# Performance work log

Hardware: AMD Instinct MI355X
Metric: run time of the kernel (lower is better)

## Reference

```python
import jax, jax.numpy as jnp
import numpy as np
import math


def _mirror_even(x):
    # even-symmetric extension: [..., H, W] -> [..., 2H, 2W]
    x = jnp.concatenate([x, jnp.flip(x, -1)], axis=-1)
    return jnp.concatenate([x, jnp.flip(x, -2)], axis=-2)


def _grad_img(x):
    # Fourier-domain spectral gradient on the even-symmetric extension,
    # matching PoissonCompositionLayer.grad_img (wx = arange(1,2W+1)-(W+1) = arange(-W,W)).
    H, W = x.shape[-2], x.shape[-1]
    kx = jnp.arange(-W, W)[None, :]          # [1, 2W]
    ky = jnp.arange(-H, H)[:, None]          # [2H, 1]
    dft = jnp.fft.fftshift(jnp.fft.fft2(_mirror_even(x)), axes=(-1, -2))
    gx = jnp.fft.ifft2(jnp.fft.fftshift((2j * math.pi / (2 * W)) * kx * dft, axes=(-1, -2))).real
    gy = jnp.fft.ifft2(jnp.fft.fftshift((2j * math.pi / (2 * H)) * ky * dft, axes=(-1, -2))).real
    return gx[..., :H, :W], gy[..., :H, :W]


def setup_inputs() -> dict:
    key = jax.random.key(0)
    k1, k2, k3 = jax.random.split(key, 3)
    B, C, H, W = 2, 3, 512, 512
    target = jax.random.normal(k1, (B, C, H, W), dtype=jnp.float32)
    source = jax.random.normal(k2, (B, C, H, W), dtype=jnp.float32)
    mask = jax.random.uniform(k3, (B, C, H, W), dtype=jnp.float32)
    return {"target": target, "source": source, "mask": mask}


def reference(target, source, mask):
    H, W = target.shape[-2], target.shape[-1]
    # composite gradient field
    gxt, gyt = _grad_img(target)
    gxs, gys = _grad_img(source)
    gx = (1.0 - mask) * gxt + mask * gxs
    gy = (1.0 - mask) * gyt + mask * gys
    # odd extension in x / even in y for gx; odd in y / even in x for gy
    gxp = jnp.concatenate([gx, -jnp.flip(gx, -1)], axis=-1)
    gxp = jnp.concatenate([gxp, jnp.flip(gxp, -2)], axis=-2)
    gyp = jnp.concatenate([gy, -jnp.flip(gy, -2)], axis=-2)
    gyp = jnp.concatenate([gyp, jnp.flip(gyp, -1)], axis=-1)
    dx = jnp.fft.fftshift(jnp.fft.fft2(gxp), axes=(-1, -2))
    dy = jnp.fft.fftshift(jnp.fft.fft2(gyp), axes=(-1, -2))
    # shifted frequency grids (DC sits at index [H, W])
    kx = jnp.arange(-W, W)[None, :]
    ky = jnp.arange(-H, H)[:, None]
    fx = 2j * math.pi * kx / (2 * W)
    fy = 2j * math.pi * ky / (2 * H)
    coeff = (fx * dx + fy * dy) / (fx ** 2 + fy ** 2 + 1e-10)
    coeff = coeff.at[..., H, W].set(0.0)  # zero DC component
    u = jnp.fft.ifft2(jnp.fft.fftshift(coeff, axes=(-1, -2)))
    res = u.real[..., :H, :W]
    # mean-matching on the unmasked region; original uses batch index 0's means for all batches
    inv = 1.0 - mask
    denom = jnp.sum(inv, axis=(-1, -2))                       # [B, C]
    mean1 = jnp.sum(target * inv, axis=(-1, -2)) / denom      # [B, C]
    mean2 = jnp.sum(res * inv, axis=(-1, -2)) / denom         # [B, C]
    return res + (mean1[0] - mean2[0])[None, :, None, None]
```

## Files before the change

kernel.cpp:

```cpp
#include <hip/hip_runtime.h>


#define CH 262144
#define NCH 6
#define NTOT (NCH*CH)

typedef _Float16 f16x8 __attribute__((ext_vector_type(8)));
typedef float f32x4  __attribute__((ext_vector_type(4)));

static constexpr float kPi        = 3.14159265358979323846f;
static constexpr float kPiOver512 = 0.006135923151542565f;
static constexpr float kPi2Norm   = 3.7649933338155804e-05f;
static constexpr float kInvHW     = 3.814697265625e-06f;

__device__ __forceinline__ void hst(float v, short* p) {
    *reinterpret_cast<_Float16*>(p) = (_Float16)v;
}

__device__ __forceinline__ float hfun(int k) {
    if (k == 0) return 0.f;
    float sgn = 1.f;
    if (k < 0) { k = -k; sgn = -1.f; }
    if (k > 512) { k = 1024 - k; sgn = -sgn; }
    float sv, cv;
    sincosf((float)k * (kPi / 1024.0f), &sv, &cv);
    float v = cv / sv;
    if (k & 1) v = -v;
    return sgn * v;
}

__device__ __forceinline__ void gl_lds16(const short* g, const short* l) {
    __builtin_amdgcn_global_load_lds(
        (const __attribute__((address_space(1))) void*)g,
        (__attribute__((address_space(3))) void*)l, 16, 0, 0);
}

#define FOFF(r, j) (((r) << 6) + 8 * ((j) ^ ((r) & 7)))
#define MFMA16(a, b, c) __builtin_amdgcn_mfma_f32_16x16x32_f16(a, b, c, 0, 0, 0)

template<int OM, int TA>
__global__ __launch_bounds__(256) void gemm_tn(
    const short* __restrict__ T0, const short* __restrict__ X0, int sX0,
    float* __restrict__ Cf0, short* __restrict__ O0, int sC0,
    const short* __restrict__ T1, const short* __restrict__ X1, int sX1,
    float* __restrict__ Cf1, short* __restrict__ O1, int sC1,
    int zsplit, const float* __restrict__ msk, float* __restrict__ redp)
{
    __shared__ short LS[2][4352];
    int z = blockIdx.z;
    const short *T, *X; float* Cf; short* O;
    if (z < zsplit) {
        T = T0; X = X0 + (size_t)z * sX0;
        Cf = Cf0 ? Cf0 + (size_t)z * sC0 : nullptr;
        O  = O0 ? O0 + (size_t)z * sC0 : nullptr;
    } else {
        int zz = z - zsplit;
        T = T1; X = X1 + (size_t)zz * sX1;
        Cf = Cf1 ? Cf1 + (size_t)zz * sC1 : nullptr;
        O  = O1 ? O1 + (size_t)zz * sC1 : nullptr;
    }
    int tid = threadIdx.x;
    int l = tid & 63, w = tid >> 6;
    int m0 = blockIdx.y * 64, n0 = blockIdx.x * 64;

    int xbase = TA ? n0 : m0;
    int srow = w * 8 + (l >> 3);
    int skc  = (l & 7) ^ ((l >> 3) & 7);
    const short* gX = X + (size_t)(xbase + srow) * 512 + 8 * skc;

    int wr = w >> 1, wc = w & 1;
    int lr = l & 15, lc = l >> 4;
    int rX0 = (TA ? wc : wr) * 32 + lr, rX1 = rX0 + 16;
    int ttb = (TA ? (m0 + wr * 32) : (n0 + wc * 32)) >> 4;
    const short* Tw0 = T + (size_t)ttb * 8192 + l * 8;
    const short* Tw1 = Tw0 + 8192;

    f32x4 a00 = {0,0,0,0}, a01 = a00, a10 = a00, a11 = a00;

#define STAGE_X(nb, k0) \
    gl_lds16(gX + (k0), &LS[nb][w * 512]); \
    gl_lds16(gX + (k0) + 32 * 512, &LS[nb][w * 512 + 2048]);

    STAGE_X(0, 0)
    __syncthreads();

    for (int step = 0; step < 8; ++step) {
        int buf = step & 1;
        if (step < 7) { STAGE_X(buf ^ 1, (step + 1) * 64) }
#pragma unroll
        for (int ks = 0; ks < 2; ++ks) {
            int j = lc + 4 * ks;
            int kc = step * 2 + ks;
            f16x8 xf0 = *(const f16x8*)&LS[buf][FOFF(rX0, j)];
            f16x8 xf1 = *(const f16x8*)&LS[buf][FOFF(rX1, j)];
            f16x8 tf0 = *(const f16x8*)(Tw0 + kc * 512);
            f16x8 tf1 = *(const f16x8*)(Tw1 + kc * 512);
            if constexpr (TA) {
                a00 = MFMA16(tf0, xf0, a00);
                a01 = MFMA16(tf0, xf1, a01);
                a10 = MFMA16(tf1, xf0, a10);
                a11 = MFMA16(tf1, xf1, a11);
            } else {
                a00 = MFMA16(xf0, tf0, a00);
                a01 = MFMA16(xf0, tf1, a01);
                a10 = MFMA16(xf1, tf0, a10);
                a11 = MFMA16(xf1, tf1, a11);
            }
        }
        __syncthreads();
    }
#undef STAGE_X

    int crow = m0 + wr * 32 + lc * 4;
    int ccol = n0 + wc * 32 + lr;
    const f32x4* accs[2][2] = {{&a00, &a01}, {&a10, &a11}};
    float lsum = 0.f;
#pragma unroll
    for (int q = 0; q < 2; ++q)
#pragma unroll
        for (int pp = 0; pp < 2; ++pp)
#pragma unroll
            for (int rr = 0; rr < 4; ++rr) {
                int idx = (crow + q * 16 + rr) * 512 + ccol + pp * 16;
                float v = (*accs[q][pp])[rr];
                if (OM == 1) {
                    hst(v, O + idx);
                } else {
                    Cf[idx] = v;
                    lsum += v * (1.0f - msk[(size_t)z * CH + idx]);
                }
            }
    if (OM == 2) {
        float* red = (float*)LS;
        red[tid] = lsum;
        __syncthreads();
        for (int s2 = 128; s2 > 0; s2 >>= 1) {
            if (tid < s2) red[tid] += red[tid + s2];
            __syncthreads();
        }
        if (tid == 0) redp[z * 64 + blockIdx.y * 8 + blockIdx.x] = red[0];
    }
}

__global__ __launch_bounds__(256) void gemm_l1(
    const short* __restrict__ dn, const short* __restrict__ dt,
    const short* __restrict__ GT, const float* __restrict__ msk,
    short* __restrict__ C_, short* __restrict__ D_)
{
    __shared__ short LS[2][4352];
    int z = blockIdx.z;
    bool gxp = z < 6;
    int zz = gxp ? z : z - 6;
    const short* X = (gxp ? dn : dt) + (size_t)zz * CH;
    const float* mz = msk + (size_t)zz * CH;

    int tid = threadIdx.x;
    int l = tid & 63, w = tid >> 6;
    int m0 = blockIdx.y * 64, n0 = blockIdx.x * 64;

    int srow = w * 8 + (l >> 3);
    int skc  = (l & 7) ^ ((l >> 3) & 7);
    const short* gX = X + (size_t)(m0 + srow) * 512 + 8 * skc;

    int wr = w >> 1, wc = w & 1;
    int lr = l & 15, lc = l >> 4;
    int rX0 = wr * 32 + lr, rX1 = rX0 + 16;
    int ttb = (n0 + wc * 32) >> 4;
    const short* Tw0 = GT + (size_t)ttb * 8192 + l * 8;
    const short* Tw1 = Tw0 + 8192;

    f32x4 a00 = {0,0,0,0}, a01 = a00, a10 = a00, a11 = a00;

#define STAGE_X(nb, k0) \
    gl_lds16(gX + (k0), &LS[nb][w * 512]); \
    gl_lds16(gX + (k0) + 32 * 512, &LS[nb][w * 512 + 2048]);

    STAGE_X(0, 0)
    __syncthreads();

    for (int step = 0; step < 8; ++step) {
        int buf = step & 1;
        if (step < 7) { STAGE_X(buf ^ 1, (step + 1) * 64) }
#pragma unroll
        for (int ks = 0; ks < 2; ++ks) {
            int j = lc + 4 * ks;
            int kc = step * 2 + ks;
            f16x8 xf0 = *(const f16x8*)&LS[buf][FOFF(rX0, j)];
            f16x8 xf1 = *(const f16x8*)&LS[buf][FOFF(rX1, j)];
            f16x8 tf0 = *(const f16x8*)(Tw0 + kc * 512);
            f16x8 tf1 = *(const f16x8*)(Tw1 + kc * 512);
            a00 = MFMA16(xf0, tf0, a00);
            a01 = MFMA16(xf0, tf1, a01);
            a10 = MFMA16(xf1, tf0, a10);
            a11 = MFMA16(xf1, tf1, a11);
        }
        __syncthreads();
    }
#undef STAGE_X

    const f32x4* accs[2][2] = {{&a00, &a01}, {&a10, &a11}};
    float* tile = (float*)LS;

    if (gxp) {
        short* o = C_ + (size_t)zz * CH;
#pragma unroll
        for (int q = 0; q < 2; ++q)
#pragma unroll
            for (int pp = 0; pp < 2; ++pp)
#pragma unroll
                for (int rr = 0; rr < 4; ++rr) {
                    int r = wr * 32 + lc * 4 + q * 16 + rr;
                    int c = wc * 32 + pp * 16 + lr;
                    float v = (*accs[q][pp])[rr] * mz[(size_t)(m0 + r) * 512 + n0 + c];
                    tile[c * 65 + r] = v;
                }
        __syncthreads();
#pragma unroll
        for (int pass = 0; pass < 16; ++pass) {
            int jj = pass * 4 + (tid >> 6);
            int ii = tid & 63;
            hst(tile[jj * 65 + ii], o + (n0 + jj) * 512 + m0 + ii);
        }
    } else {
        short* o = D_ + (size_t)zz * CH;
#pragma unroll
        for (int pass = 0; pass < 16; ++pass) {
            int ii = pass * 4 + (tid >> 6);
            int jj = tid & 63;
            tile[jj * 65 + ii] = mz[(size_t)(n0 + ii) * 512 + m0 + jj];
        }
        __syncthreads();
#pragma unroll
        for (int q = 0; q < 2; ++q)
#pragma unroll
            for (int pp = 0; pp < 2; ++pp)
#pragma unroll
                for (int rr = 0; rr < 4; ++rr) {
                    int r = wr * 32 + lc * 4 + q * 16 + rr;
                    int c = wc * 32 + pp * 16 + lr;
                    float v = (*accs[q][pp])[rr] * tile[r * 65 + c];
                    hst(v, o + (m0 + r) * 512 + n0 + c);
                }
    }
}

__global__ __launch_bounds__(256) void gemm_l3(
    const short* __restrict__ Ms, const short* __restrict__ Mc,
    const short* __restrict__ P, const short* __restrict__ Q,
    short* __restrict__ O_)
{
    __shared__ short LS[2][2][4096];
    int z = blockIdx.z;
    const short* pz = P + (size_t)z * CH;
    const short* qz = Q + (size_t)z * CH;
    short* o = O_ + (size_t)z * CH;

    int tid = threadIdx.x;
    int l = tid & 63, w = tid >> 6;
    int m0 = blockIdx.y * 64, n0 = blockIdx.x * 64;

    int srow = w * 8 + (l >> 3);
    int skc  = (l & 7) ^ ((l >> 3) & 7);
    const short* gP = pz + (size_t)(n0 + srow) * 512 + 8 * skc;
    const short* gQ = qz + (size_t)(n0 + srow) * 512 + 8 * skc;

    int wr = w >> 1, wc = w & 1;
    int lr = l & 15, lc = l >> 4;
    int rB0 = wc * 32 + lr, rB1 = rB0 + 16;
    int ttb = (m0 + wr * 32) >> 4;
    const short* ms0p = Ms + (size_t)ttb * 8192 + l * 8;
    const short* ms1p = ms0p + 8192;
    const short* mc0p = Mc + (size_t)ttb * 8192 + l * 8;
    const short* mc1p = mc0p + 8192;

    f32x4 x00 = {0,0,0,0}, x01 = x00, x10 = x00, x11 = x00;
    f32x4 y00 = x00, y01 = x00, y10 = x00, y11 = x00;

#define STAGE_PQ(nb, k0) \
    gl_lds16(gP + (k0), &LS[nb][0][w * 512]); \
    gl_lds16(gP + (k0) + 32 * 512, &LS[nb][0][w * 512 + 2048]); \
    gl_lds16(gQ + (k0), &LS[nb][1][w * 512]); \
    gl_lds16(gQ + (k0) + 32 * 512, &LS[nb][1][w * 512 + 2048]);

    STAGE_PQ(0, 0)
    __syncthreads();

    for (int step = 0; step < 8; ++step) {
        int buf = step & 1;
        if (step < 7) { STAGE_PQ(buf ^ 1, (step + 1) * 64) }
#pragma unroll
        for (int ks = 0; ks < 2; ++ks) {
            int j = lc + 4 * ks;
            int kc = step * 2 + ks;
            f16x8 p0 = *(const f16x8*)&LS[buf][0][FOFF(rB0, j)];
            f16x8 p1 = *(const f16x8*)&LS[buf][0][FOFF(rB1, j)];
            f16x8 s0 = *(const f16x8*)(ms0p + kc * 512);
            f16x8 s1 = *(const f16x8*)(ms1p + kc * 512);
            x00 = MFMA16(s0, p0, x00);
            x01 = MFMA16(s0, p1, x01);
            x10 = MFMA16(s1, p0, x10);
            x11 = MFMA16(s1, p1, x11);
            f16x8 q0 = *(const f16x8*)&LS[buf][1][FOFF(rB0, j)];
            f16x8 q1 = *(const f16x8*)&LS[buf][1][FOFF(rB1, j)];
            f16x8 c0 = *(const f16x8*)(mc0p + kc * 512);
            f16x8 c1 = *(const f16x8*)(mc1p + kc * 512);
            y00 = MFMA16(c0, q0, y00);
            y01 = MFMA16(c0, q1, y01);
            y10 = MFMA16(c1, q0, y10);
            y11 = MFMA16(c1, q1, y11);
        }
        __syncthreads();
    }
#undef STAGE_PQ

    int crow = m0 + wr * 32 + lc * 4;
    int ccol = n0 + wc * 32 + lr;
    const f32x4* xs[2][2] = {{&x00, &x01}, {&x10, &x11}};
    const f32x4* ys[2][2] = {{&y00, &y01}, {&y10, &y11}};
#pragma unroll
    for (int q = 0; q < 2; ++q)
#pragma unroll
        for (int pp = 0; pp < 2; ++pp) {
            int u = ccol + pp * 16;
            float eu = (u ? 2.0f : 1.0f) * kInvHW;
#pragma unroll
            for (int rr = 0; rr < 4; ++rr) {
                int v = crow + q * 16 + rr;
                float gx = (*xs[q][pp])[rr];
                float gy = (*ys[q][pp])[rr];
                float num = kPiOver512 * ((float)v * gx + (float)u * gy);
                float den = 1e-10f - kPi2Norm * (float)(u * u + v * v);
                float eps = (v ? 2.0f : 1.0f) * eu;
                hst(eps * num / den, o + v * 512 + u);
            }
        }
}

__global__ __launch_bounds__(256) void diff_split_tab(
    const float* __restrict__ s, const float* __restrict__ t, const float* __restrict__ m,
    short* __restrict__ dn, short* __restrict__ dt,
    short* __restrict__ Mc, short* __restrict__ Ms,
    short* __restrict__ McT, short* __restrict__ GT,
    float* __restrict__ mt, float* __restrict__ mi)
{
    int z = blockIdx.z;
    if (z == 6) {
        int bid = blockIdx.y * 16 + blockIdx.x;
        if (bid >= 128) return;
        int g = bid * 256 + threadIdx.x;
        int f = g >> 6, lane = g & 63;
        int r  = ((f >> 4) << 4) | (lane & 15);
        int kb = ((f & 15) << 5) | ((lane >> 4) << 3);
        f16x8 vmc, vms, vmct, vgt;
#pragma unroll
        for (int e = 0; e < 8; ++e) {
            int k = kb + e;
            int p1 = (r * (2 * k + 1)) & 2047;
            float s1, c1; sincosf((float)p1 * (kPi / 1024.0f), &s1, &c1);
            int p2 = (k * (2 * r + 1)) & 2047;
            float s2, c2; sincosf((float)p2 * (kPi / 1024.0f), &s2, &c2);
            float gt = (kPi / 1024.0f) * (hfun(r + k + 1) + hfun(r - k));
            vmc[e]  = (_Float16)c1;
            vms[e]  = (_Float16)s1;
            vmct[e] = (_Float16)c2;
            vgt[e]  = (_Float16)gt;
        }
        *(f16x8*)(Mc  + (size_t)g * 8) = vmc;
        *(f16x8*)(Ms  + (size_t)g * 8) = vms;
        *(f16x8*)(McT + (size_t)g * 8) = vmct;
        *(f16x8*)(GT  + (size_t)g * 8) = vgt;
        return;
    }

    __shared__ float tile[32][33];
    __shared__ float red[512];
    const float* sz = s + (size_t)z * CH;
    const float* tz = t + (size_t)z * CH;
    const float* mz = m + (size_t)z * CH;
    short* nh = dn + (size_t)z * CH;
    short* th = dt + (size_t)z * CH;
    int bx = blockIdx.x * 32, by = blockIdx.y * 32;
    int tx = threadIdx.x & 31, ty = threadIdx.x >> 5;
    float accT = 0.f, accI = 0.f;
    for (int r = ty; r < 32; r += 8) {
        int idx = (by + r) * 512 + bx + tx;
        float tv = tz[idx];
        float d = sz[idx] - tv;
        tile[r][tx] = d;
        hst(d, nh + idx);
        accT += tv;
        if (z < 3) accI += 1.0f - mz[idx];
    }
    __syncthreads();
    for (int r = ty; r < 32; r += 8) {
        hst(tile[tx][r], th + (bx + r) * 512 + by + tx);
    }
    int tid = threadIdx.x;
    red[tid] = accT; red[256 + tid] = accI;
    __syncthreads();
    for (int s2 = 128; s2 > 0; s2 >>= 1) {
        if (tid < s2) { red[tid] += red[tid + s2]; red[256 + tid] += red[256 + tid + s2]; }
        __syncthreads();
    }
    if (tid == 0) {
        int tileid = blockIdx.y * 16 + blockIdx.x;
        mt[z * 256 + tileid] = red[0];
        if (z < 3) mi[z * 256 + tileid] = red[256];
    }
}

__global__ __launch_bounds__(256) void final_out(
    const float* __restrict__ t, const float* __restrict__ U,
    const float* __restrict__ part, float* __restrict__ out)
{
    __shared__ float mtv[6], wmuv[3];
    int tid = threadIdx.x;
    if (tid < 6) {
        float s2 = 0.f;
        for (int k = 0; k < 256; ++k) s2 += part[tid * 256 + k];
        mtv[tid] = s2 * (1.0f / (float)CH);
    }
    if (tid >= 8 && tid < 11) {
        int c = tid - 8;
        float si = 0.f, su = 0.f;
        for (int k = 0; k < 256; ++k) si += part[1536 + c * 256 + k];
        for (int k = 0; k < 64; ++k) su += part[2304 + c * 64 + k];
        wmuv[c] = su / si;
    }
    __syncthreads();
    int n4 = NTOT / 4;
    for (int i = blockIdx.x * blockDim.x + tid; i < n4; i += gridDim.x * blockDim.x) {
        int z = i >> 16;
        int c = z % 3;
        float sh = -mtv[z] + mtv[c] - wmuv[c];
        float4 tv = ((const float4*)t)[i];
        float4 uv = ((const float4*)U)[i];
        ((float4*)out)[i] = make_float4(tv.x + uv.x + sh, tv.y + uv.y + sh,
                                        tv.z + uv.z + sh, tv.w + uv.w + sh);
    }
}

extern "C" void kernel_launch(void* const* d_in, const int* in_sizes, int n_in,
                              void* d_out, int out_size, void* d_ws, size_t ws_size,
                              hipStream_t stream) {
    const float* t = (const float*)d_in[0];
    const float* s = (const float*)d_in[1];
    const float* m = (const float*)d_in[2];
    float* out = (float*)d_out;
    float* F = (float*)d_ws;
    if (ws_size < (size_t)(21 * CH + 4096) * sizeof(float)) return;

    short* T = (short*)F;
    short *Mc = T, *Ms = T + (size_t)CH, *McT = T + 2 * (size_t)CH, *GT = T + 3 * (size_t)CH;
    short* A_ = (short*)(F + 2  * (size_t)CH);
    short* B_ = (short*)(F + 5  * (size_t)CH);
    short* C_ = (short*)(F + 8  * (size_t)CH);
    short* D_ = (short*)(F + 11 * (size_t)CH);
    float* F0  = F + 14 * (size_t)CH;
    float* part = F + 20 * (size_t)CH;

    diff_split_tab<<<dim3(16, 16, 7), 256, 0, stream>>>(s, t, m, A_, B_,
                                                        Mc, Ms, McT, GT,
                                                        part, part + 1536);

    gemm_l1<<<dim3(8, 8, 12), 256, 0, stream>>>(A_, B_, GT, m, C_, D_);

    gemm_tn<1, 1><<<dim3(8, 8, 12), 256, 0, stream>>>(
        Mc, C_, CH, nullptr, A_, CH,
        Ms, D_, CH, nullptr, B_, CH, 6, nullptr, nullptr);

    gemm_l3<<<dim3(8, 8, 6), 256, 0, stream>>>(Ms, Mc, A_, B_, C_);

    gemm_tn<1, 1><<<dim3(8, 8, 6), 256, 0, stream>>>(
        McT, C_, CH, nullptr, D_, CH,
        McT, C_, CH, nullptr, D_, CH, 6, nullptr, nullptr);

    gemm_tn<2, 0><<<dim3(8, 8, 6), 256, 0, stream>>>(
        McT, D_, CH, F0, nullptr, CH,
        McT, D_, CH, F0, nullptr, CH, 6, m, part + 2304);

    final_out<<<768, 256, 0, stream>>>(t, F0, part, out);
}
```

Baseline: 77.95 us.

## Prefetch twiddle fragments one step ahead and remap blocks across XCDs

In the three MFMA GEMM kernels, the global loads of the constant transform-matrix fragments move one K-step ahead into registers, so they overlap with the current step's MFMAs instead of sitting in the critical path. The step loop is also fully unrolled. A new XCD-aware block remap reassigns linear workgroup IDs so consecutive tiles land on the same XCD, which should improve L2 reuse of shared operands. The cost is higher register pressure from the extra prefetch registers. The LDS buffer in gemm_tn also shrinks slightly.

```diff
diff --git a/kernel.cpp b/kernel.cpp
--- a/kernel.cpp
+++ b/kernel.cpp
@@ -29,6 +29,16 @@
     return sgn * v;
 }
 
+__device__ __forceinline__ void xcd_remap(int& bx, int& by, int& bz) {
+    int nx = gridDim.x, ny = gridDim.y;
+    int nwg = nx * ny * gridDim.z;
+    int w = blockIdx.x + nx * (blockIdx.y + ny * blockIdx.z);
+    int s = (w & 7) * (nwg >> 3) + (w >> 3);
+    bx = s % nx; s /= nx;
+    by = s % ny;
+    bz = s / ny;
+}
+
 __device__ __forceinline__ void gl_lds16(const short* g, const short* l) {
     __builtin_amdgcn_global_load_lds(
         (const __attribute__((address_space(1))) void*)g,
@@ -46,8 +56,9 @@
     float* __restrict__ Cf1, short* __restrict__ O1, int sC1,
     int zsplit, const float* __restrict__ msk, float* __restrict__ redp)
 {
-    __shared__ short LS[2][4352];
-    int z = blockIdx.z;
+    __shared__ short LS[2][4096];
+    int bx, by, z;
+    xcd_remap(bx, by, z);
     const short *T, *X; float* Cf; short* O;
     if (z < zsplit) {
         T = T0; X = X0 + (size_t)z * sX0;
@@ -61,7 +72,7 @@
     }
     int tid = threadIdx.x;
     int l = tid & 63, w = tid >> 6;
-    int m0 = blockIdx.y * 64, n0 = blockIdx.x * 64;
+    int m0 = by * 64, n0 = bx * 64;
 
     int xbase = TA ? n0 : m0;
     int srow = w * 8 + (l >> 3);
@@ -82,32 +93,57 @@
     gl_lds16(gX + (k0) + 32 * 512, &LS[nb][w * 512 + 2048]);
 
     STAGE_X(0, 0)
+    f16x8 ct00 = *(const f16x8*)(Tw0);
+    f16x8 ct01 = *(const f16x8*)(Tw0 + 512);
+    f16x8 ct10 = *(const f16x8*)(Tw1);
+    f16x8 ct11 = *(const f16x8*)(Tw1 + 512);
     __syncthreads();
 
+#pragma unroll
     for (int step = 0; step < 8; ++step) {
         int buf = step & 1;
-        if (step < 7) { STAGE_X(buf ^ 1, (step + 1) * 64) }
-#pragma unroll
-        for (int ks = 0; ks < 2; ++ks) {
-            int j = lc + 4 * ks;
-            int kc = step * 2 + ks;
-            f16x8 xf0 = *(const f16x8*)&LS[buf][FOFF(rX0, j)];
-            f16x8 xf1 = *(const f16x8*)&LS[buf][FOFF(rX1, j)];
-            f16x8 tf0 = *(const f16x8*)(Tw0 + kc * 512);
-            f16x8 tf1 = *(const f16x8*)(Tw1 + kc * 512);
+        f16x8 nt00, nt01, nt10, nt11;
+        if (step < 7) {
+            STAGE_X(buf ^ 1, (step + 1) * 64)
+            const short* tn0 = Tw0 + (2 * step + 2) * 512;
+            const short* tn1 = Tw1 + (2 * step + 2) * 512;
+            nt00 = *(const f16x8*)(tn0);
+            nt01 = *(const f16x8*)(tn0 + 512);
+            nt10 = *(const f16x8*)(tn1);
+            nt11 = *(const f16x8*)(tn1 + 512);
+        }
+        {
+            f16x8 x0 = *(const f16x8*)&LS[buf][FOFF(rX0, lc)];
+            f16x8 x1 = *(const f16x8*)&LS[buf][FOFF(rX1, lc)];
             if constexpr (TA) {
-                a00 = MFMA16(tf0, xf0, a00);
-                a01 = MFMA16(tf0, xf1, a01);
-                a10 = MFMA16(tf1, xf0, a10);
-                a11 = MFMA16(tf1, xf1, a11);
+                a00 = MFMA16(ct00, x0, a00);
+                a01 = MFMA16(ct00, x1, a01);
+                a10 = MFMA16(ct10, x0, a10);
+                a11 = MFMA16(ct10, x1, a11);
             } else {
-                a00 = MFMA16(xf0, tf0, a00);
-                a01 = MFMA16(xf0, tf1, a01);
-                a10 = MFMA16(xf1, tf0, a10);
-                a11 = MFMA16(xf1, tf1, a11);
+                a00 = MFMA16(x0, ct00, a00);
+                a01 = MFMA16(x0, ct10, a01);
+                a10 = MFMA16(x1, ct00, a10);
+                a11 = MFMA16(x1, ct10, a11);
             }
         }
-        __syncthreads();
+        {
+            f16x8 x0 = *(const f16x8*)&LS[buf][FOFF(rX0, lc + 4)];
+            f16x8 x1 = *(const f16x8*)&LS[buf][FOFF(rX1, lc + 4)];
+            if constexpr (TA) {
+                a00 = MFMA16(ct01, x0, a00);
+                a01 = MFMA16(ct01, x1, a01);
+                a10 = MFMA16(ct11, x0, a10);
+                a11 = MFMA16(ct11, x1, a11);
+            } else {
+                a00 = MFMA16(x0, ct01, a00);
+                a01 = MFMA16(x0, ct11, a01);
+                a10 = MFMA16(x1, ct01, a10);
+                a11 = MFMA16(x1, ct11, a11);
+            }
+        }
+        __syncthreads();
+        if (step < 7) { ct00 = nt00; ct01 = nt01; ct10 = nt10; ct11 = nt11; }
     }
 #undef STAGE_X
 
@@ -138,7 +174,7 @@
             if (tid < s2) red[tid] += red[tid + s2];
             __syncthreads();
         }
-        if (tid == 0) redp[z * 64 + blockIdx.y * 8 + blockIdx.x] = red[0];
+        if (tid == 0) redp[z * 64 + by * 8 + bx] = red[0];
     }
 }
 
@@ -148,7 +184,8 @@
     short* __restrict__ C_, short* __restrict__ D_)
 {
     __shared__ short LS[2][4352];
-    int z = blockIdx.z;
+    int bx, by, z;
+    xcd_remap(bx, by, z);
     bool gxp = z < 6;
     int zz = gxp ? z : z - 6;
     const short* X = (gxp ? dn : dt) + (size_t)zz * CH;
@@ -156,7 +193,7 @@
 
     int tid = threadIdx.x;
     int l = tid & 63, w = tid >> 6;
-    int m0 = blockIdx.y * 64, n0 = blockIdx.x * 64;
+    int m0 = by * 64, n0 = bx * 64;
 
     int srow = w * 8 + (l >> 3);
     int skc  = (l & 7) ^ ((l >> 3) & 7);
@@ -176,25 +213,43 @@
     gl_lds16(gX + (k0) + 32 * 512, &LS[nb][w * 512 + 2048]);
 
     STAGE_X(0, 0)
+    f16x8 ct00 = *(const f16x8*)(Tw0);
+    f16x8 ct01 = *(const f16x8*)(Tw0 + 512);
+    f16x8 ct10 = *(const f16x8*)(Tw1);
+    f16x8 ct11 = *(const f16x8*)(Tw1 + 512);
     __syncthreads();
 
+#pragma unroll
     for (int step = 0; step < 8; ++step) {
         int buf = step & 1;
-        if (step < 7) { STAGE_X(buf ^ 1, (step + 1) * 64) }
-#pragma unroll
-        for (int ks = 0; ks < 2; ++ks) {
-            int j = lc + 4 * ks;
-            int kc = step * 2 + ks;
-            f16x8 xf0 = *(const f16x8*)&LS[buf][FOFF(rX0, j)];
-            f16x8 xf1 = *(const f16x8*)&LS[buf][FOFF(rX1, j)];
-            f16x8 tf0 = *(const f16x8*)(Tw0 + kc * 512);
-            f16x8 tf1 = *(const f16x8*)(Tw1 + kc * 512);
-            a00 = MFMA16(xf0, tf0, a00);
-            a01 = MFMA16(xf0, tf1, a01);
-            a10 = MFMA16(xf1, tf0, a10);
-            a11 = MFMA16(xf1, tf1, a11);
-        }
-        __syncthreads();
+        f16x8 nt00, nt01, nt10, nt11;
+        if (step < 7) {
+            STAGE_X(buf ^ 1, (step + 1) * 64)
+            const short* tn0 = Tw0 + (2 * step + 2) * 512;
+            const short* tn1 = Tw1 + (2 * step + 2) * 512;
+            nt00 = *(const f16x8*)(tn0);
+            nt01 = *(const f16x8*)(tn0 + 512);
+            nt10 = *(const f16x8*)(tn1);
+            nt11 = *(const f16x8*)(tn1 + 512);
+        }
+        {
+            f16x8 x0 = *(const f16x8*)&LS[buf][FOFF(rX0, lc)];
+            f16x8 x1 = *(const f16x8*)&LS[buf][FOFF(rX1, lc)];
+            a00 = MFMA16(x0, ct00, a00);
+            a01 = MFMA16(x0, ct10, a01);
+            a10 = MFMA16(x1, ct00, a10);
+            a11 = MFMA16(x1, ct10, a11);
+        }
+        {
+            f16x8 x0 = *(const f16x8*)&LS[buf][FOFF(rX0, lc + 4)];
+            f16x8 x1 = *(const f16x8*)&LS[buf][FOFF(rX1, lc + 4)];
+            a00 = MFMA16(x0, ct01, a00);
+            a01 = MFMA16(x0, ct11, a01);
+            a10 = MFMA16(x1, ct01, a10);
+            a11 = MFMA16(x1, ct11, a11);
+        }
+        __syncthreads();
+        if (step < 7) { ct00 = nt00; ct01 = nt01; ct10 = nt10; ct11 = nt11; }
     }
 #undef STAGE_X
 
@@ -250,14 +305,15 @@
     short* __restrict__ O_)
 {
     __shared__ short LS[2][2][4096];
-    int z = blockIdx.z;
+    int bx, by, z;
+    xcd_remap(bx, by, z);
     const short* pz = P + (size_t)z * CH;
     const short* qz = Q + (size_t)z * CH;
     short* o = O_ + (size_t)z * CH;
 
     int tid = threadIdx.x;
     int l = tid & 63, w = tid >> 6;
-    int m0 = blockIdx.y * 64, n0 = blockIdx.x * 64;
+    int m0 = by * 64, n0 = bx * 64;
 
     int srow = w * 8 + (l >> 3);
     int skc  = (l & 7) ^ ((l >> 3) & 7);
@@ -268,10 +324,10 @@
     int lr = l & 15, lc = l >> 4;
     int rB0 = wc * 32 + lr, rB1 = rB0 + 16;
     int ttb = (m0 + wr * 32) >> 4;
-    const short* ms0p = Ms + (size_t)ttb * 8192 + l * 8;
-    const short* ms1p = ms0p + 8192;
-    const short* mc0p = Mc + (size_t)ttb * 8192 + l * 8;
-    const short* mc1p = mc0p + 8192;
+    const short* Sw0 = Ms + (size_t)ttb * 8192 + l * 8;
+    const short* Sw1 = Sw0 + 8192;
+    const short* Cw0 = Mc + (size_t)ttb * 8192 + l * 8;
+    const short* Cw1 = Cw0 + 8192;
 
     f32x4 x00 = {0,0,0,0}, x01 = x00, x10 = x00, x11 = x00;
     f32x4 y00 = x00, y01 = x00, y10 = x00, y11 = x00;
@@ -283,33 +339,65 @@
     gl_lds16(gQ + (k0) + 32 * 512, &LS[nb][1][w * 512 + 2048]);
 
     STAGE_PQ(0, 0)
+    f16x8 cs00 = *(const f16x8*)(Sw0);
+    f16x8 cs01 = *(const f16x8*)(Sw0 + 512);
+    f16x8 cs10 = *(const f16x8*)(Sw1);
+    f16x8 cs11 = *(const f16x8*)(Sw1 + 512);
+    f16x8 cc00 = *(const f16x8*)(Cw0);
+    f16x8 cc01 = *(const f16x8*)(Cw0 + 512);
+    f16x8 cc10 = *(const f16x8*)(Cw1);
+    f16x8 cc11 = *(const f16x8*)(Cw1 + 512);
     __syncthreads();
 
+#pragma unroll
     for (int step = 0; step < 8; ++step) {
         int buf = step & 1;
-        if (step < 7) { STAGE_PQ(buf ^ 1, (step + 1) * 64) }
-#pragma unroll
-        for (int ks = 0; ks < 2; ++ks) {
-            int j = lc + 4 * ks;
-            int kc = step * 2 + ks;
-            f16x8 p0 = *(const f16x8*)&LS[buf][0][FOFF(rB0, j)];
-            f16x8 p1 = *(const f16x8*)&LS[buf][0][FOFF(rB1, j)];
-            f16x8 s0 = *(const f16x8*)(ms0p + kc * 512);
-            f16x8 s1 = *(const f16x8*)(ms1p + kc * 512);
-            x00 = MFMA16(s0, p0, x00);
-            x01 = MFMA16(s0, p1, x01);
-            x10 = MFMA16(s1, p0, x10);
-            x11 = MFMA16(s1, p1, x11);
-            f16x8 q0 = *(const f16x8*)&LS[buf][1][FOFF(rB0, j)];
-            f16x8 q1 = *(const f16x8*)&LS[buf][1][FOFF(rB1, j)];
-            f16x8 c0 = *(const f16x8*)(mc0p + kc * 512);
-            f16x8 c1 = *(const f16x8*)(mc1p + kc * 512);
-            y00 = MFMA16(c0, q0, y00);
-            y01 = MFMA16(c0, q1, y01);
-            y10 = MFMA16(c1, q0, y10);
-            y11 = MFMA16(c1, q1, y11);
-        }
-        __syncthreads();
+        f16x8 ns00, ns01, ns10, ns11, nc00, nc01, nc10, nc11;
+        if (step < 7) {
+            STAGE_PQ(buf ^ 1, (step + 1) * 64)
+            int kc = (2 * step + 2) * 512;
+            ns00 = *(const f16x8*)(Sw0 + kc);
+            ns01 = *(const f16x8*)(Sw0 + kc + 512);
+            ns10 = *(const f16x8*)(Sw1 + kc);
+            ns11 = *(const f16x8*)(Sw1 + kc + 512);
+            nc00 = *(const f16x8*)(Cw0 + kc);
+            nc01 = *(const f16x8*)(Cw0 + kc + 512);
+            nc10 = *(const f16x8*)(Cw1 + kc);
+            nc11 = *(const f16x8*)(Cw1 + kc + 512);
+        }
+        {
+            f16x8 p0 = *(const f16x8*)&LS[buf][0][FOFF(rB0, lc)];
+            f16x8 p1 = *(const f16x8*)&LS[buf][0][FOFF(rB1, lc)];
+            x00 = MFMA16(cs00, p0, x00);
+            x01 = MFMA16(cs00, p1, x01);
+            x10 = MFMA16(cs10, p0, x10);
+            x11 = MFMA16(cs10, p1, x11);
+            f16x8 q0 = *(const f16x8*)&LS[buf][1][FOFF(rB0, lc)];
+            f16x8 q1 = *(const f16x8*)&LS[buf][1][FOFF(rB1, lc)];
+            y00 = MFMA16(cc00, q0, y00);
+            y01 = MFMA16(cc00, q1, y01);
+            y10 = MFMA16(cc10, q0, y10);
+            y11 = MFMA16(cc10, q1, y11);
+        }
+        {
+            f16x8 p0 = *(const f16x8*)&LS[buf][0][FOFF(rB0, lc + 4)];
+            f16x8 p1 = *(const f16x8*)&LS[buf][0][FOFF(rB1, lc + 4)];
+            x00 = MFMA16(cs01, p0, x00);
+            x01 = MFMA16(cs01, p1, x01);
+            x10 = MFMA16(cs11, p0, x10);
+            x11 = MFMA16(cs11, p1, x11);
+            f16x8 q0 = *(const f16x8*)&LS[buf][1][FOFF(rB0, lc + 4)];
+            f16x8 q1 = *(const f16x8*)&LS[buf][1][FOFF(rB1, lc + 4)];
+            y00 = MFMA16(cc01, q0, y00);
+            y01 = MFMA16(cc01, q1, y01);
+            y10 = MFMA16(cc11, q0, y10);
+            y11 = MFMA16(cc11, q1, y11);
+        }
+        __syncthreads();
+        if (step < 7) {
+            cs00 = ns00; cs01 = ns01; cs10 = ns10; cs11 = ns11;
+            cc00 = nc00; cc01 = nc01; cc10 = nc10; cc11 = nc11;
+        }
     }
 #undef STAGE_PQ
 
```

New measurement: 72.19 us. 1.08x faster.
